# Optimization experiments

Hardware: AMD Instinct MI355X
Metric: run time of the kernel (lower is better)

The kernel has to match this reference:

```python
import jax, jax.numpy as jnp
import numpy as np
from jax import lax

NMS_THRESH = 0.5      # IoU threshold 'thresh' in the torch forward
MAX_PROPOSALS = 1000  # 'max_proposals' in the torch forward


def setup_inputs() -> dict:
    key = jax.random.key(0)
    k1, k2, k3 = jax.random.split(key, 3)
    N = 10000
    # realistic xyxy boxes inside a ~1000x1000 image
    centers = jax.random.uniform(k1, (N, 2), dtype=jnp.float32) * 1000.0
    wh = jax.random.uniform(k2, (N, 2), dtype=jnp.float32) * 99.0 + 1.0
    boxes = jnp.concatenate([centers - wh / 2.0, centers + wh / 2.0], axis=-1)  # [N,4]
    scores = jax.random.uniform(k3, (N,), dtype=jnp.float32)  # [N]
    return {"boxes": boxes, "scores": scores}


def _pairwise_iou(b):
    # b: [N,4] xyxy, sorted by score. Returns [N,N] IoU matrix.
    x1, y1, x2, y2 = b[:, 0], b[:, 1], b[:, 2], b[:, 3]
    areas = (x2 - x1) * (y2 - y1)                      # [N]
    ix1 = jnp.maximum(x1[:, None], x1[None, :])
    iy1 = jnp.maximum(y1[:, None], y1[None, :])
    ix2 = jnp.minimum(x2[:, None], x2[None, :])
    iy2 = jnp.minimum(y2[:, None], y2[None, :])
    iw = jnp.maximum(ix2 - ix1, 0.0)
    ih = jnp.maximum(iy2 - iy1, 0.0)
    inter = iw * ih                                    # [N,N]
    union = areas[:, None] + areas[None, :] - inter
    return inter / jnp.maximum(union, 1e-9)


def reference(boxes, scores):
    # Faithful greedy NMS: sort by score desc, suppress lower-scored boxes
    # with IoU > thresh against any kept higher-scored box.
    N = boxes.shape[0]
    order = jnp.argsort(-scores)
    b = boxes[order]        # [N,4] score-sorted
    s = scores[order]       # [N]
    ious = _pairwise_iou(b)  # [N,N]
    idx = jnp.arange(N)

    def body(i, keep):
        # if box i is still kept, suppress all later boxes overlapping it
        suppress = keep[i] & (ious[i] > NMS_THRESH) & (idx > i)
        return keep & ~suppress

    keep = lax.fori_loop(0, N, body, jnp.ones((N,), dtype=bool))
    # keep = keep[:max_proposals] in the torch code: first MAX_PROPOSALS kept boxes
    rank = jnp.cumsum(keep.astype(jnp.int32)) - 1
    keep = keep & (rank < MAX_PROPOSALS)
    # fixed-shape equivalent of boxlist[keep]: zero out suppressed entries
    boxes_out = jnp.where(keep[:, None], b, 0.0)   # [N,4]
    scores_out = jnp.where(keep, s, 0.0)           # [N]
    return boxes_out, scores_out, keep
```

## Files before the change

### kernel.cpp

```cpp
#include <hip/hip_runtime.h>
#include <stdint.h>

#define MAX_PROPOSALS 1000
#define WPAD 160
#define JCH 16
#define NSTRIPE 128
#define SCAP 2048
#define LDSE 13312
#define G 10
#define NCELL (G * G)

__global__ __launch_bounds__(256) void k_rank(const float* __restrict__ scores,
                                              int* __restrict__ rank2d,
                                              int* __restrict__ ecnt,
                                              int* __restrict__ cellCnt, int N) {
  if (blockIdx.x == 0 && blockIdx.y == 0) {
    if (threadIdx.x < NSTRIPE) ecnt[threadIdx.x] = 0;
    if (threadIdx.x < NCELL) cellCnt[threadIdx.x] = 0;
  }
  int jc = blockIdx.y;
  int chunk = (N + JCH - 1) / JCH;
  int j0 = jc * chunk;
  int j1 = min(N, j0 + chunk);
  extern __shared__ uint64_t shk[];
  for (int j = j0 + threadIdx.x; j < j1; j += 256) {
    uint32_t b = __float_as_uint(scores[j]);
    shk[j - j0] = ((uint64_t)b << 32) | (uint64_t)(0xFFFFFFFFu - (uint32_t)j);
  }
  __syncthreads();
  int i = blockIdx.x * 256 + threadIdx.x;
  if (i >= N) return;
  uint64_t ki = ((uint64_t)__float_as_uint(scores[i]) << 32) | (uint64_t)(0xFFFFFFFFu - (uint32_t)i);
  int r = 0;
  int j = j0;
  for (; j + 4 <= j1; j += 4) {
    uint64_t A = shk[j - j0], B = shk[j - j0 + 1], C = shk[j - j0 + 2], D = shk[j - j0 + 3];
    r += (A > ki);
    r += (B > ki);
    r += (C > ki);
    r += (D > ki);
  }
  for (; j < j1; ++j) r += (shk[j - j0] > ki);
  rank2d[(size_t)jc * N + i] = r;
}

__device__ __forceinline__ int cell_of(float lo, float hi) {
  int g = (int)((lo + hi) * 0.005f);
  return min(max(g, 0), G - 1);
}

__global__ __launch_bounds__(256) void k_scatter(const float4* __restrict__ boxes,
                       const float* __restrict__ scores, const int* __restrict__ rank2d,
                       float4* __restrict__ sbox, float* __restrict__ ss,
                       int* __restrict__ cellCnt, int N) {
  int i = blockIdx.x * 256 + threadIdx.x;
  if (i >= N) return;
  int r = 0;
  #pragma unroll
  for (int c = 0; c < JCH; ++c) r += rank2d[(size_t)c * N + i];
  float4 b = boxes[i];
  sbox[r] = b;
  ss[r]   = scores[i];
  int cell = cell_of(b.y, b.w) * G + cell_of(b.x, b.z);
  atomicAdd(&cellCnt[cell], 1);
}

__global__ __launch_bounds__(1024) void k_cellbuild(const float4* __restrict__ sbox,
                       const int* __restrict__ cellCnt, int* __restrict__ cellStart,
                       float4* __restrict__ sboxC, int* __restrict__ cellRank, int N) {
  __shared__ int curs[NCELL];
  int tid = threadIdx.x;
  if (tid < 64) {
    int l = tid;
    int a = (2 * l < NCELL) ? cellCnt[2 * l] : 0;
    int b = (2 * l + 1 < NCELL) ? cellCnt[2 * l + 1] : 0;
    int s = a + b, inc = s;
    #pragma unroll
    for (int d = 1; d < 64; d <<= 1) {
      int v = __shfl_up(inc, d, 64);
      if (l >= d) inc += v;
    }
    int ex = inc - s;
    if (2 * l < NCELL)     { cellStart[2 * l] = ex;         curs[2 * l] = ex; }
    if (2 * l + 1 < NCELL) { cellStart[2 * l + 1] = ex + a; curs[2 * l + 1] = ex + a; }
    if (l == 63) cellStart[NCELL] = inc;
  }
  __syncthreads();
  for (int r = tid; r < N; r += 1024) {
    float4 b = sbox[r];
    int cell = cell_of(b.y, b.w) * G + cell_of(b.x, b.z);
    int pos = atomicAdd(&curs[cell], 1);
    sboxC[pos] = b;
    cellRank[pos] = r;
  }
}

__global__ __launch_bounds__(256) void k_maskR2(const float4* __restrict__ sbox,
                        const int* __restrict__ cellStart,
                        const float4* __restrict__ sboxC, const int* __restrict__ cellRank,
                        uint32_t* __restrict__ edges, int* __restrict__ ecnt, int N) {
  int wv = threadIdx.x >> 6, lane = threadIdx.x & 63;
  int i = blockIdx.x * 4 + wv;
  if (i >= N) return;
  int stripe = blockIdx.x & (NSTRIPE - 1);
  uint32_t* estr = edges + (size_t)stripe * SCAP;

  float4 iB = sbox[i];
  float iar = (iB.z - iB.x) * (iB.w - iB.y);
  int cx = cell_of(iB.x, iB.z), cy = cell_of(iB.y, iB.w);
  int x0 = max(cx - 1, 0), x1 = min(cx + 1, G - 1);
  int y0 = max(cy - 1, 0), y1 = min(cy + 1, G - 1);

  for (int ry = y0; ry <= y1; ++ry) {
    int s = cellStart[ry * G + x0];
    int e = cellStart[ry * G + x1 + 1];
    if (s >= e) continue;

    int p = s + lane;
    int pc = (p < e) ? p : s;
    float4 cB = sboxC[pc];
    int rk = cellRank[pc];

    for (int p0 = s; p0 < e; p0 += 64) {
      float4 curB = cB;
      int currk = rk;
      bool curv = (p0 + lane) < e;

      if (p0 + 64 < e) {
        int np = p0 + 64 + lane;
        int npc = (np < e) ? np : s;
        cB = sboxC[npc];
        rk = cellRank[npc];
      }

      float car = (curB.z - curB.x) * (curB.w - curB.y);
      float ix1 = fmaxf(iB.x, curB.x);
      float iy1 = fmaxf(iB.y, curB.y);
      float ix2 = fminf(iB.z, curB.z);
      float iy2 = fminf(iB.w, curB.w);
      float iw = fmaxf(ix2 - ix1, 0.0f);
      float ih = fmaxf(iy2 - iy1, 0.0f);
      float inter = iw * ih;
      float uni = (iar + car) - inter;
      float m_ = fmaxf(uni, 1e-9f);
      float t_ = 0.5f * m_;
      bool pred = (inter > t_) && curv && (currk > i);
      bool ambig = pred && (inter <= t_ + t_ * 3e-7f);
      if (__builtin_expect(__ballot(ambig) != 0ull, 0)) {
        if (ambig) pred = (inter / m_) > 0.5f;
      }
      uint64_t ball = __ballot(pred);
      if (__builtin_expect(ball != 0ull, 0)) {
        int cnt = __popcll(ball);
        int base = 0;
        if (lane == 0) base = atomicAdd(&ecnt[stripe], cnt);
        base = __shfl(base, 0, 64);
        if (pred) {
          int pos = base + __popcll(ball & ((1ull << lane) - 1ull));
          if (pos < SCAP) estr[pos] = ((uint32_t)i << 14) | (uint32_t)currk;
        }
      }
    }
  }
}

__global__ __launch_bounds__(1024) void k_scanJ(const uint32_t* __restrict__ edges,
                                                const int* __restrict__ ecnt,
                                                const float4* __restrict__ sbox,
                                                const float* __restrict__ ss,
                                                float* __restrict__ out, int N) {
  const int tid = threadIdx.x, l = tid & 63, wave = tid >> 6;
  const int nw = (N + 63) >> 6;
  const int nh = 2 * nw;

  __shared__ uint32_t eL[LDSE];
  __shared__ int scnt[NSTRIPE], soff[NSTRIPE];
  __shared__ int eTot;
  __shared__ uint32_t kc[2 * WPAD];
  __shared__ uint32_t kn[2 * WPAD];
  __shared__ uint32_t baseL[2 * WPAD];
  __shared__ uint64_t keepL[WPAD];
  __shared__ int wprefL[WPAD];
  __shared__ int chgS;

  if (wave == 0) {
    int a = min(ecnt[2 * l], SCAP);
    int b = min(ecnt[2 * l + 1], SCAP);
    int s = a + b, inc = s;
    #pragma unroll
    for (int d = 1; d < 64; d <<= 1) {
      int v = __shfl_up(inc, d, 64);
      if (l >= d) inc += v;
    }
    int ex = inc - s;
    scnt[2 * l] = a;     soff[2 * l] = ex;
    scnt[2 * l + 1] = b; soff[2 * l + 1] = ex + a;
    if (l == 63) eTot = min(inc, LDSE);
  }
  for (int w = tid; w < 2 * WPAD; w += 1024) {
    long lo = (long)(w >> 1) * 64 + (long)(w & 1) * 32;
    long rem = (long)N - lo;
    uint32_t m = (rem >= 32) ? 0xFFFFFFFFu : ((rem <= 0) ? 0u : ((1u << rem) - 1u));
    baseL[w] = m;
    kc[w] = m;
  }
  __syncthreads();

  for (int s = wave; s < NSTRIPE; s += 16) {
    int cnt = scnt[s], off = soff[s];
    const uint32_t* src = edges + (size_t)s * SCAP;
    for (int k = l; k < cnt; k += 64) {
      int dst = off + k;
      if (dst < LDSE) eL[dst] = src[k];
    }
  }
  __syncthreads();
  int EL = eTot;

  for (int round = 0; round < 10001; ++round) {
    for (int w = tid; w < nh; w += 1024) kn[w] = baseL[w];
    if (tid == 0) chgS = 0;
    __syncthreads();

    for (int e = tid; e < EL; e += 1024) {
      uint32_t p = eL[e];
      int i = (int)(p >> 14);
      int j = (int)(p & 0x3FFFu);
      if ((kc[i >> 5] >> (i & 31)) & 1u)
        atomicAnd(&kn[j >> 5], ~(1u << (j & 31)));
    }
    __syncthreads();

    int local = 0;
    for (int w = tid; w < nh; w += 1024) {
      uint32_t a = kn[w];
      if (a != kc[w]) local = 1;
      kc[w] = a;
    }
    if (local) chgS = 1;
    __syncthreads();
    bool done = (chgS == 0);
    __syncthreads();
    if (done) break;
  }

  for (int i = tid; i < WPAD; i += 1024)
    keepL[i] = (i < nw) ? (((uint64_t)kc[2 * i + 1] << 32) | (uint64_t)kc[2 * i]) : 0ull;
  __syncthreads();

  if (wave == 0) {
    uint64_t k0 = keepL[l], k1 = keepL[64 + l];
    uint64_t k2v = (128 + l < WPAD) ? keepL[128 + l] : 0ull;
    int p0 = __popcll(k0), p1 = __popcll(k1), p2 = __popcll(k2v);
    int s0 = p0, s1 = p1, s2 = p2;
    #pragma unroll
    for (int d = 1; d < 64; d <<= 1) {
      int v0 = __shfl_up(s0, d, 64), v1 = __shfl_up(s1, d, 64), v2 = __shfl_up(s2, d, 64);
      if (l >= d) { s0 += v0; s1 += v1; s2 += v2; }
    }
    int tot0 = __shfl(s0, 63, 64);
    int tot1 = __shfl(s1, 63, 64);
    wprefL[l] = s0 - p0;
    wprefL[64 + l] = tot0 + s1 - p1;
    if (128 + l < WPAD) wprefL[128 + l] = tot0 + tot1 + s2 - p2;
  }
  __syncthreads();

  float4* bo = (float4*)out;
  float* so = out + (size_t)4 * N;
  float* ko = so + N;
  for (int i = tid; i < N; i += 1024) {
    int w = i >> 6, b = i & 63;
    uint64_t kwv = keepL[w];
    bool kept = (kwv >> b) & 1ull;
    int rank = wprefL[w] + __popcll(kwv & ((1ull << b) - 1ull));
    bool fin = kept && (rank < MAX_PROPOSALS);
    float4 bx = sbox[i];
    if (!fin) { bx.x = 0.0f; bx.y = 0.0f; bx.z = 0.0f; bx.w = 0.0f; }
    bo[i] = bx;
    so[i] = fin ? ss[i] : 0.0f;
    ko[i] = fin ? 1.0f : 0.0f;
  }
}

extern "C" void kernel_launch(void* const* d_in, const int* in_sizes, int n_in,
                              void* d_out, int out_size, void* d_ws, size_t ws_size,
                              hipStream_t stream) {
  const float* boxes  = (const float*)d_in[0];
  const float* scores = (const float*)d_in[1];
  int N = in_sizes[1];

  char* ws = (char*)d_ws;
  size_t off = 0;
  float4* sbox = (float4*)(ws + off); off += (size_t)N * 16;
  float4* sboxC = (float4*)(ws + off); off += (size_t)N * 16;
  float* ss    = (float*)(ws + off);  off += (size_t)N * 4;
  int* cellRank = (int*)(ws + off); off += (size_t)N * 4;
  off = (off + 255) & ~(size_t)255;
  int* rank2d = (int*)(ws + off); off += (size_t)JCH * N * 4;
  off = (off + 255) & ~(size_t)255;
  uint32_t* edges = (uint32_t*)(ws + off); off += (size_t)NSTRIPE * SCAP * 4;
  int* ecnt = (int*)(ws + off); off += NSTRIPE * 4;
  int* cellCnt   = (int*)(ws + off); off += NCELL * 4;
  int* cellStart = (int*)(ws + off); off += (NCELL + 1) * 4;

  int nblk = (N + 255) / 256;
  int chunk = (N + JCH - 1) / JCH;

  k_rank<<<dim3(nblk, JCH), 256, (size_t)chunk * sizeof(uint64_t), stream>>>(scores, rank2d, ecnt, cellCnt, N);
  k_scatter<<<nblk, 256, 0, stream>>>((const float4*)boxes, scores, rank2d, sbox, ss, cellCnt, N);
  k_cellbuild<<<1, 1024, 0, stream>>>(sbox, cellCnt, cellStart, sboxC, cellRank, N);
  k_maskR2<<<(N + 3) / 4, 256, 0, stream>>>(sbox, cellStart, sboxC, cellRank, edges, ecnt, N);
  k_scanJ<<<1, 1024, 0, stream>>>(edges, ecnt, sbox, ss, (float*)d_out, N);
}
```

Measured before the change: 135.0 us.

## Replace O(N^2) rank sort with bucketed score sort and parallel output stage

Replaces the all-pairs rank computation (16 chunked blocks comparing every key) with a 4096-bucket histogram, prefix scan, bucket scatter and in-bucket rank counting, so sorting cost scales with bucket occupancy instead of N. The cell binning is folded into the rank-scatter kernel, which removes the single-block cellbuild pass. The final output write moves from the single-block scan kernel into a separate grid-wide kernel. This adds kernel launches (zero, hist, prefix, bscatter, rankscatter, out), relies on scores being roughly uniform in [0,1) for balanced buckets, and makes cell order within a cell nondeterministic.

After: 121.6 us, median of 2. 9.9% less time.

```diff
diff --git a/kernel.cpp b/kernel.cpp
--- a/kernel.cpp
+++ b/kernel.cpp
@@ -3,96 +3,119 @@
 
 #define MAX_PROPOSALS 1000
 #define WPAD 160
-#define JCH 16
 #define NSTRIPE 128
 #define SCAP 2048
 #define LDSE 13312
 #define G 10
 #define NCELL (G * G)
-
-__global__ __launch_bounds__(256) void k_rank(const float* __restrict__ scores,
-                                              int* __restrict__ rank2d,
-                                              int* __restrict__ ecnt,
-                                              int* __restrict__ cellCnt, int N) {
-  if (blockIdx.x == 0 && blockIdx.y == 0) {
-    if (threadIdx.x < NSTRIPE) ecnt[threadIdx.x] = 0;
-    if (threadIdx.x < NCELL) cellCnt[threadIdx.x] = 0;
-  }
-  int jc = blockIdx.y;
-  int chunk = (N + JCH - 1) / JCH;
-  int j0 = jc * chunk;
-  int j1 = min(N, j0 + chunk);
-  extern __shared__ uint64_t shk[];
-  for (int j = j0 + threadIdx.x; j < j1; j += 256) {
-    uint32_t b = __float_as_uint(scores[j]);
-    shk[j - j0] = ((uint64_t)b << 32) | (uint64_t)(0xFFFFFFFFu - (uint32_t)j);
-  }
-  __syncthreads();
-  int i = blockIdx.x * 256 + threadIdx.x;
-  if (i >= N) return;
-  uint64_t ki = ((uint64_t)__float_as_uint(scores[i]) << 32) | (uint64_t)(0xFFFFFFFFu - (uint32_t)i);
-  int r = 0;
-  int j = j0;
-  for (; j + 4 <= j1; j += 4) {
-    uint64_t A = shk[j - j0], B = shk[j - j0 + 1], C = shk[j - j0 + 2], D = shk[j - j0 + 3];
-    r += (A > ki);
-    r += (B > ki);
-    r += (C > ki);
-    r += (D > ki);
-  }
-  for (; j < j1; ++j) r += (shk[j - j0] > ki);
-  rank2d[(size_t)jc * N + i] = r;
-}
+#define NB 4096
 
 __device__ __forceinline__ int cell_of(float lo, float hi) {
   int g = (int)((lo + hi) * 0.005f);
   return min(max(g, 0), G - 1);
 }
-
-__global__ __launch_bounds__(256) void k_scatter(const float4* __restrict__ boxes,
-                       const float* __restrict__ scores, const int* __restrict__ rank2d,
-                       float4* __restrict__ sbox, float* __restrict__ ss,
-                       int* __restrict__ cellCnt, int N) {
+__device__ __forceinline__ int bucket_of(float s) {
+  int b = (int)(s * (float)NB);
+  return min(max(b, 0), NB - 1);
+}
+
+__global__ __launch_bounds__(1024) void k_zero(int* __restrict__ p, int n) {
+  for (int i = threadIdx.x; i < n; i += 1024) p[i] = 0;
+}
+
+__global__ __launch_bounds__(256) void k_hist(const float* __restrict__ scores,
+                                              const float4* __restrict__ boxes,
+                                              int* __restrict__ hist,
+                                              int* __restrict__ cellCnt, int N) {
   int i = blockIdx.x * 256 + threadIdx.x;
   if (i >= N) return;
-  int r = 0;
-  #pragma unroll
-  for (int c = 0; c < JCH; ++c) r += rank2d[(size_t)c * N + i];
+  float s = scores[i];
+  atomicAdd(&hist[bucket_of(s)], 1);
   float4 b = boxes[i];
-  sbox[r] = b;
-  ss[r]   = scores[i];
   int cell = cell_of(b.y, b.w) * G + cell_of(b.x, b.z);
   atomicAdd(&cellCnt[cell], 1);
 }
 
-__global__ __launch_bounds__(1024) void k_cellbuild(const float4* __restrict__ sbox,
-                       const int* __restrict__ cellCnt, int* __restrict__ cellStart,
-                       float4* __restrict__ sboxC, int* __restrict__ cellRank, int N) {
-  __shared__ int curs[NCELL];
-  int tid = threadIdx.x;
-  if (tid < 64) {
-    int l = tid;
+__global__ __launch_bounds__(1024) void k_prefix(const int* __restrict__ hist,
+                       int* __restrict__ bstart, int* __restrict__ bcur,
+                       const int* __restrict__ cellCnt,
+                       int* __restrict__ cellStart, int* __restrict__ cellCur) {
+  __shared__ int wsum[16];
+  int tid = threadIdx.x, l = tid & 63, wv = tid >> 6;
+  int h[4];
+  int base4 = tid * 4;
+  int s = 0;
+  #pragma unroll
+  for (int k = 0; k < 4; ++k) { h[k] = hist[base4 + k]; s += h[k]; }
+  int inc = s;
+  #pragma unroll
+  for (int d = 1; d < 64; d <<= 1) {
+    int v = __shfl_up(inc, d, 64);
+    if (l >= d) inc += v;
+  }
+  if (l == 63) wsum[wv] = inc;
+  __syncthreads();
+  if (tid == 0) {
+    int run = 0;
+    for (int w = 0; w < 16; ++w) { int v = wsum[w]; wsum[w] = run; run += v; }
+  }
+  __syncthreads();
+  int ex = wsum[wv] + inc - s;
+  #pragma unroll
+  for (int k = 0; k < 4; ++k) { bstart[base4 + k] = ex; bcur[base4 + k] = ex; ex += h[k]; }
+  if (tid == 1023) bstart[NB] = ex;
+
+  if (wv == 0) {
     int a = (2 * l < NCELL) ? cellCnt[2 * l] : 0;
     int b = (2 * l + 1 < NCELL) ? cellCnt[2 * l + 1] : 0;
-    int s = a + b, inc = s;
+    int s2 = a + b, inc2 = s2;
     #pragma unroll
     for (int d = 1; d < 64; d <<= 1) {
-      int v = __shfl_up(inc, d, 64);
-      if (l >= d) inc += v;
-    }
-    int ex = inc - s;
-    if (2 * l < NCELL)     { cellStart[2 * l] = ex;         curs[2 * l] = ex; }
-    if (2 * l + 1 < NCELL) { cellStart[2 * l + 1] = ex + a; curs[2 * l + 1] = ex + a; }
-    if (l == 63) cellStart[NCELL] = inc;
-  }
-  __syncthreads();
-  for (int r = tid; r < N; r += 1024) {
-    float4 b = sbox[r];
-    int cell = cell_of(b.y, b.w) * G + cell_of(b.x, b.z);
-    int pos = atomicAdd(&curs[cell], 1);
-    sboxC[pos] = b;
-    cellRank[pos] = r;
-  }
+      int v = __shfl_up(inc2, d, 64);
+      if (l >= d) inc2 += v;
+    }
+    int ex2 = inc2 - s2;
+    if (2 * l < NCELL)     { cellStart[2 * l] = ex2;         cellCur[2 * l] = ex2; }
+    if (2 * l + 1 < NCELL) { cellStart[2 * l + 1] = ex2 + a; cellCur[2 * l + 1] = ex2 + a; }
+    if (l == 63) cellStart[NCELL] = inc2;
+  }
+}
+
+__global__ __launch_bounds__(256) void k_bscatter(const float* __restrict__ scores,
+                       int* __restrict__ bcur, uint64_t* __restrict__ bkey,
+                       int* __restrict__ bidx, int N) {
+  int i = blockIdx.x * 256 + threadIdx.x;
+  if (i >= N) return;
+  float s = scores[i];
+  uint64_t key = ((uint64_t)__float_as_uint(s) << 32) | (uint64_t)(0xFFFFFFFFu - (uint32_t)i);
+  int b = bucket_of(s);
+  int pos = atomicAdd(&bcur[b], 1);
+  bkey[pos] = key;
+  bidx[pos] = i;
+}
+
+__global__ __launch_bounds__(256) void k_rankscatter(const uint64_t* __restrict__ bkey,
+                       const int* __restrict__ bidx, const int* __restrict__ bstart,
+                       const float4* __restrict__ boxes,
+                       int* __restrict__ cellCur,
+                       float4* __restrict__ sbox, float* __restrict__ ss,
+                       float4* __restrict__ sboxC, int* __restrict__ cellRank, int N) {
+  int p = blockIdx.x * 256 + threadIdx.x;
+  if (p >= N) return;
+  uint64_t key = bkey[p];
+  float s = __uint_as_float((uint32_t)(key >> 32));
+  int b = bucket_of(s);
+  int q0 = bstart[b], q1 = bstart[b + 1];
+  int r = N - q1;
+  for (int q = q0; q < q1; ++q) r += (bkey[q] > key);
+  int idx = bidx[p];
+  float4 bx = boxes[idx];
+  sbox[r] = bx;
+  ss[r] = s;
+  int cell = cell_of(bx.y, bx.w) * G + cell_of(bx.x, bx.z);
+  int cpos = atomicAdd(&cellCur[cell], 1);
+  sboxC[cpos] = bx;
+  cellRank[cpos] = r;
 }
 
 __global__ __launch_bounds__(256) void k_maskR2(const float4* __restrict__ sbox,
@@ -166,9 +189,8 @@
 
 __global__ __launch_bounds__(1024) void k_scanJ(const uint32_t* __restrict__ edges,
                                                 const int* __restrict__ ecnt,
-                                                const float4* __restrict__ sbox,
-                                                const float* __restrict__ ss,
-                                                float* __restrict__ out, int N) {
+                                                uint64_t* __restrict__ keepw,
+                                                int* __restrict__ wpref, int N) {
   const int tid = threadIdx.x, l = tid & 63, wave = tid >> 6;
   const int nw = (N + 63) >> 6;
   const int nh = 2 * nw;
@@ -180,7 +202,6 @@
   __shared__ uint32_t kn[2 * WPAD];
   __shared__ uint32_t baseL[2 * WPAD];
   __shared__ uint64_t keepL[WPAD];
-  __shared__ int wprefL[WPAD];
   __shared__ int chgS;
 
   if (wave == 0) {
@@ -260,56 +281,73 @@
     }
     int tot0 = __shfl(s0, 63, 64);
     int tot1 = __shfl(s1, 63, 64);
-    wprefL[l] = s0 - p0;
-    wprefL[64 + l] = tot0 + s1 - p1;
-    if (128 + l < WPAD) wprefL[128 + l] = tot0 + tot1 + s2 - p2;
-  }
-  __syncthreads();
-
-  float4* bo = (float4*)out;
-  float* so = out + (size_t)4 * N;
-  float* ko = so + N;
-  for (int i = tid; i < N; i += 1024) {
-    int w = i >> 6, b = i & 63;
-    uint64_t kwv = keepL[w];
-    bool kept = (kwv >> b) & 1ull;
-    int rank = wprefL[w] + __popcll(kwv & ((1ull << b) - 1ull));
-    bool fin = kept && (rank < MAX_PROPOSALS);
-    float4 bx = sbox[i];
-    if (!fin) { bx.x = 0.0f; bx.y = 0.0f; bx.z = 0.0f; bx.w = 0.0f; }
-    bo[i] = bx;
-    so[i] = fin ? ss[i] : 0.0f;
-    ko[i] = fin ? 1.0f : 0.0f;
-  }
+    keepw[l] = k0;
+    keepw[64 + l] = k1;
+    if (128 + l < WPAD) keepw[128 + l] = k2v;
+    wpref[l] = s0 - p0;
+    wpref[64 + l] = tot0 + s1 - p1;
+    if (128 + l < WPAD) wpref[128 + l] = tot0 + tot1 + s2 - p2;
+  }
+}
+
+__global__ __launch_bounds__(256) void k_out(const float4* __restrict__ sbox,
+                      const float* __restrict__ ss,
+                      const uint64_t* __restrict__ keepw, const int* __restrict__ wpref,
+                      float* __restrict__ out, int N) {
+  int i = blockIdx.x * 256 + threadIdx.x;
+  if (i >= N) return;
+  int w = i >> 6, b = i & 63;
+  uint64_t kw = keepw[w];
+  bool kept = (kw >> b) & 1ull;
+  int rank = wpref[w] + __popcll(kw & ((1ull << b) - 1ull));
+  bool fin = kept && (rank < MAX_PROPOSALS);
+  float4 bx = sbox[i];
+  if (!fin) { bx.x = 0.0f; bx.y = 0.0f; bx.z = 0.0f; bx.w = 0.0f; }
+  ((float4*)out)[i] = bx;
+  out[(size_t)4 * N + i] = fin ? ss[i] : 0.0f;
+  out[(size_t)5 * N + i] = fin ? 1.0f : 0.0f;
 }
 
 extern "C" void kernel_launch(void* const* d_in, const int* in_sizes, int n_in,
                               void* d_out, int out_size, void* d_ws, size_t ws_size,
                               hipStream_t stream) {
-  const float* boxes  = (const float*)d_in[0];
+  const float4* boxes = (const float4*)d_in[0];
   const float* scores = (const float*)d_in[1];
   int N = in_sizes[1];
 
   char* ws = (char*)d_ws;
   size_t off = 0;
-  float4* sbox = (float4*)(ws + off); off += (size_t)N * 16;
+  int* hist    = (int*)(ws + off); off += NB * 4;
+  int* ecnt    = (int*)(ws + off); off += NSTRIPE * 4;
+  int* cellCnt = (int*)(ws + off); off += NCELL * 4;
+  int zints = NB + NSTRIPE + NCELL;
+  off = (off + 255) & ~(size_t)255;
+  int* bstart   = (int*)(ws + off); off += (NB + 1) * 4;
+  int* bcur     = (int*)(ws + off); off += NB * 4;
+  int* cellStart= (int*)(ws + off); off += (NCELL + 1) * 4;
+  int* cellCur  = (int*)(ws + off); off += NCELL * 4;
+  off = (off + 255) & ~(size_t)255;
+  uint64_t* bkey = (uint64_t*)(ws + off); off += (size_t)N * 8;
+  int* bidx      = (int*)(ws + off); off += (size_t)N * 4;
+  off = (off + 255) & ~(size_t)255;
+  float4* sbox  = (float4*)(ws + off); off += (size_t)N * 16;
   float4* sboxC = (float4*)(ws + off); off += (size_t)N * 16;
-  float* ss    = (float*)(ws + off);  off += (size_t)N * 4;
+  float* ss     = (float*)(ws + off);  off += (size_t)N * 4;
   int* cellRank = (int*)(ws + off); off += (size_t)N * 4;
   off = (off + 255) & ~(size_t)255;
-  int* rank2d = (int*)(ws + off); off += (size_t)JCH * N * 4;
-  off = (off + 255) & ~(size_t)255;
   uint32_t* edges = (uint32_t*)(ws + off); off += (size_t)NSTRIPE * SCAP * 4;
-  int* ecnt = (int*)(ws + off); off += NSTRIPE * 4;
-  int* cellCnt   = (int*)(ws + off); off += NCELL * 4;
-  int* cellStart = (int*)(ws + off); off += (NCELL + 1) * 4;
+  uint64_t* keepw = (uint64_t*)(ws + off); off += WPAD * 8;
+  int* wpref      = (int*)(ws + off); off += WPAD * 4;
 
   int nblk = (N + 255) / 256;
-  int chunk = (N + JCH - 1) / JCH;
-
-  k_rank<<<dim3(nblk, JCH), 256, (size_t)chunk * sizeof(uint64_t), stream>>>(scores, rank2d, ecnt, cellCnt, N);
-  k_scatter<<<nblk, 256, 0, stream>>>((const float4*)boxes, scores, rank2d, sbox, ss, cellCnt, N);
-  k_cellbuild<<<1, 1024, 0, stream>>>(sbox, cellCnt, cellStart, sboxC, cellRank, N);
+
+  k_zero<<<1, 1024, 0, stream>>>(hist, zints);
+  k_hist<<<nblk, 256, 0, stream>>>(scores, boxes, hist, cellCnt, N);
+  k_prefix<<<1, 1024, 0, stream>>>(hist, bstart, bcur, cellCnt, cellStart, cellCur);
+  k_bscatter<<<nblk, 256, 0, stream>>>(scores, bcur, bkey, bidx, N);
+  k_rankscatter<<<nblk, 256, 0, stream>>>(bkey, bidx, bstart, boxes, cellCur,
+                                          sbox, ss, sboxC, cellRank, N);
   k_maskR2<<<(N + 3) / 4, 256, 0, stream>>>(sbox, cellStart, sboxC, cellRank, edges, ecnt, N);
-  k_scanJ<<<1, 1024, 0, stream>>>(edges, ecnt, sbox, ss, (float*)d_out, N);
-}
+  k_scanJ<<<1, 1024, 0, stream>>>(edges, ecnt, keepw, wpref, N);
+  k_out<<<nblk, 256, 0, stream>>>(sbox, ss, keepw, wpref, (float*)d_out, N);
+}
```
